# Kernel optimization log

Hardware: AMD Instinct MI355X
Metric: run time of the kernel (lower is better)

## Reference

```python
import jax, jax.numpy as jnp
import numpy as np

N_NODES = 50000
N_EDGES = 800000
N_GRAPHS = 64
F_IN = 128
HEADS = 4
CH = 32
HID = HEADS * CH  # 128
N_CLASSES = 10
N_LAYERS = 3
NEG_SLOPE = 0.2


def setup_inputs() -> dict:
    key = jax.random.key(0)
    ks = jax.random.split(key, 12)
    x = jax.random.normal(ks[0], (N_NODES, F_IN), dtype=jnp.float32)
    edge_index = jax.random.randint(ks[1], (2, N_EDGES), 0, N_NODES, dtype=jnp.int64)
    batch = jnp.sort(jax.random.randint(ks[2], (N_NODES,), 0, N_GRAPHS, dtype=jnp.int64))
    s = 0.1
    Wl = jax.random.normal(ks[3], (N_LAYERS, F_IN, HID), dtype=jnp.float32) * s
    Wr = jax.random.normal(ks[4], (N_LAYERS, F_IN, HID), dtype=jnp.float32) * s
    bl = jax.random.normal(ks[5], (N_LAYERS, HID), dtype=jnp.float32) * s
    br = jax.random.normal(ks[6], (N_LAYERS, HID), dtype=jnp.float32) * s
    att = jax.random.normal(ks[7], (N_LAYERS, HEADS, CH), dtype=jnp.float32) * s
    bias = jax.random.normal(ks[8], (N_LAYERS, HID), dtype=jnp.float32) * s
    lin_w = jax.random.normal(ks[9], (HID, N_CLASSES), dtype=jnp.float32) * s
    lin_b = jax.random.normal(ks[10], (N_CLASSES,), dtype=jnp.float32) * s
    return {"x": x, "edge_index": edge_index, "batch": batch, "Wl": Wl, "Wr": Wr,
            "bl": bl, "br": br, "att": att, "bias": bias, "lin_w": lin_w, "lin_b": lin_b}


def gatv2_layer(x, Wl, Wr, bl, br, att, bias, src, dst):
    # x: [N, D_in] -> out: [N, HEADS*CH]
    n = x.shape[0]
    xl = (x @ Wl + bl).reshape(n, HEADS, CH)  # source transform
    xr = (x @ Wr + br).reshape(n, HEADS, CH)  # target transform
    # GATv2 edge scores: a^T LeakyReLU(W_l x_j + W_r x_i), per head
    e = jnp.einsum('ehc,hc->eh', jax.nn.leaky_relu(xl[src] + xr[dst], NEG_SLOPE), att)  # [E, H]
    # softmax over edges sharing the same destination node
    m = jax.ops.segment_max(e, dst, num_segments=n)
    ee = jnp.exp(e - m[dst])
    denom = jax.ops.segment_sum(ee, dst, num_segments=n)
    alpha = ee / denom[dst]  # [E, H]
    out = jax.ops.segment_sum(xl[src] * alpha[:, :, None], dst, num_segments=n)  # [N, H, C]
    return out.reshape(n, HID) + bias


def reference(x, edge_index, batch, Wl, Wr, bl, br, att, bias, lin_w, lin_b):
    n = x.shape[0]
    loop = jnp.arange(n, dtype=edge_index.dtype)
    src = jnp.concatenate([edge_index[0], loop])  # self loops (PyG default)
    dst = jnp.concatenate([edge_index[1], loop])
    h = x
    for l in range(N_LAYERS):
        h = jax.nn.elu(gatv2_layer(h, Wl[l], Wr[l], bl[l], br[l], att[l], bias[l], src, dst))
    # global mean pool over graphs
    sums = jax.ops.segment_sum(h, batch, num_segments=N_GRAPHS)
    cnt = jax.ops.segment_sum(jnp.ones((n,), h.dtype), batch, num_segments=N_GRAPHS)
    pooled = sums / jnp.maximum(cnt, 1.0)[:, None]
    logits = jax.nn.elu(pooled @ lin_w + lin_b)
    return jax.nn.log_softmax(logits, axis=1)
```

## Files before the change

kernel.cpp:

```cpp
#include <hip/hip_runtime.h>
#include <hip/hip_bf16.h>
#include <math.h>

#define N_NODES 50000
#define N_EDGES 800000
#define N_GRAPHS 64
#define HID 128
#define N_CLASSES 10
#define N_LAYERS 3
#define NEG_SLOPE 0.2f

#define NB 196
#define BCAP 5120
#define ACHUNK 4096

typedef __attribute__((ext_vector_type(8))) short short8;
typedef __attribute__((ext_vector_type(4))) float f32x4;
typedef __attribute__((ext_vector_type(2))) _Float16 h2;

extern "C" __device__ _Float16 __ocml_exp2_f16(_Float16);

__device__ inline ushort f2bf(float f) {
    uint u = __builtin_bit_cast(uint, f);
    u += 0x7fffu + ((u >> 16) & 1u);
    return (ushort)(u >> 16);
}
__device__ inline uint pk2bf(float a, float b) {
    return (uint)f2bf(a) | ((uint)f2bf(b) << 16);
}
__device__ inline h2 pkh(float a, float b) {
    return __builtin_bit_cast(h2, __builtin_amdgcn_cvt_pkrtz(a, b));
}
__device__ inline uint rne8(uint h) {
    return (h + 0x7fu + ((h >> 8) & 1u)) >> 8;
}
__device__ inline uint pk4e5m2(uint h01, uint h23) {
    uint a = rne8(h01 & 0xffffu);
    uint b = rne8(h01 >> 16);
    uint c = rne8(h23 & 0xffffu);
    uint d = rne8(h23 >> 16);
    return a | (b << 8) | (c << 16) | (d << 24);
}


__global__ __launch_bounds__(256) void setup_kernel(
    const float* __restrict__ x, uint* __restrict__ xb, int n,
    const float* __restrict__ Wl, const float* __restrict__ Wr,
    uint* __restrict__ wt, int wtot,
    const int* __restrict__ ei, int E,
    int* __restrict__ bptr, uint* __restrict__ bbuf,
    int xqb, int wb) {
    __shared__ int hcnt[256];
    __shared__ int hexcl[256];
    __shared__ int lofs[256];
    __shared__ int delta[256];
    __shared__ uint stage[ACHUNK];
    int t = threadIdx.x;
    int blk = blockIdx.x;

    if (blk < xqb) {
        int j = blk * 256 + t;
        if (j < n * 16) {
            const float4* xp = (const float4*)x + (size_t)j * 2;
            float4 a = xp[0], b = xp[1];
            uint4 o;
            o.x = pk2bf(a.x, a.y); o.y = pk2bf(a.z, a.w);
            o.z = pk2bf(b.x, b.y); o.w = pk2bf(b.z, b.w);
            ((uint4*)xb)[j] = o;
        }
        return;
    }
    blk -= xqb;
    if (blk < wb) {
        int i = blk * 256 + t;
        if (i >= wtot) return;
        int kp = i & 63;
        int nn = (i >> 6) & 255;
        int l  = i >> 14;
        const float* W = (nn < 128) ? Wl : Wr;
        int c = nn & 127;
        wt[i] = pk2bf(W[l * 16384 + (2 * kp) * 128 + c],
                      W[l * 16384 + (2 * kp + 1) * 128 + c]);
        return;
    }
    blk -= wb;
    int total = E + n;
    int base = blk * ACHUNK;
    int cntblk = min(ACHUNK, total - base);
    hcnt[t] = 0; lofs[t] = 0;
    __syncthreads();

    uint v[16]; int bk[16];
#pragma unroll
    for (int j = 0; j < 16; ++j) {
        int e = base + j * 256 + t;
        bk[j] = -1;
        if (e < total) {
            int s, d;
            if (e < E) { s = ei[e]; d = ei[E + e]; }
            else       { s = e - E; d = e - E; }
            v[j] = ((uint)s << 16) | (uint)d;
            bk[j] = d >> 8;
            atomicAdd(&hcnt[bk[j]], 1);
        }
    }
    __syncthreads();
    int hv = hcnt[t];
    __shared__ int stmp[256];
    stmp[t] = hv;
    __syncthreads();
    for (int off = 1; off < 256; off <<= 1) {
        int u = (t >= off) ? stmp[t - off] : 0;
        __syncthreads();
        stmp[t] += u;
        __syncthreads();
    }
    hexcl[t] = stmp[t] - hv;
    __syncthreads();
#pragma unroll
    for (int j = 0; j < 16; ++j) {
        if (bk[j] >= 0) {
            int pos = hexcl[bk[j]] + atomicAdd(&lofs[bk[j]], 1);
            stage[pos] = v[j];
        }
    }
    __syncthreads();
    if (t < NB) {
        int c = hcnt[t];
        int gb = c ? atomicAdd(&bptr[t], c) : 0;
        delta[t] = t * BCAP + gb - hexcl[t];
    }
    __syncthreads();
    for (int idx = t; idx < cntblk; idx += 256) {
        uint val = stage[idx];
        int b = (val >> 8) & 0xff;
        int tgt = delta[b] + idx;
        if (tgt < (b + 1) * BCAP) bbuf[tgt] = val;
    }
}


__device__ __forceinline__ void gemm_body(
    const ushort* __restrict__ A, const ushort* __restrict__ Wt,
    const float* __restrict__ bl, const float* __restrict__ br,
    uchar* __restrict__ xlb, ushort* __restrict__ xrb, int n, int bid, int tid) {
    int wv = tid >> 6;
    int lane = tid & 63;
    int q = lane >> 4, m16 = lane & 15;
    int m0 = bid * 64;

    short8 bf[4][4];
#pragma unroll
    for (int nt = 0; nt < 4; ++nt) {
        const ushort* wp = Wt + (size_t)(wv * 64 + nt * 16 + m16) * 128 + q * 8;
#pragma unroll
        for (int ks = 0; ks < 4; ++ks) bf[nt][ks] = *(const short8*)(wp + ks * 32);
    }
    const ushort* ap[4];
#pragma unroll
    for (int mt = 0; mt < 4; ++mt) {
        int r = m0 + mt * 16 + m16;
        if (r > n - 1) r = n - 1;
        ap[mt] = A + (size_t)r * 128 + q * 8;
    }

    f32x4 z = {0.f, 0.f, 0.f, 0.f};
    f32x4 acc[4][4];
#pragma unroll
    for (int mt = 0; mt < 4; ++mt)
#pragma unroll
        for (int nt = 0; nt < 4; ++nt) acc[mt][nt] = z;

#pragma unroll
    for (int ks = 0; ks < 4; ++ks) {
        short8 af[4];
#pragma unroll
        for (int mt = 0; mt < 4; ++mt) af[mt] = *(const short8*)(ap[mt] + ks * 32);
#pragma unroll
        for (int mt = 0; mt < 4; ++mt)
#pragma unroll
            for (int nt = 0; nt < 4; ++nt)
                acc[mt][nt] = __builtin_amdgcn_mfma_f32_16x16x32_bf16(
                    bf[nt][ks], af[mt], acc[mt][nt], 0, 0, 0);
    }

    int fb = (wv & 1) * 64;
    if (wv >= 2) {
        const float* bx = br;
#pragma unroll
        for (int nt = 0; nt < 4; ++nt) {
            int fcol = fb + nt * 16 + q * 4;
            float4 b4 = *(const float4*)&bx[fcol];
#pragma unroll
            for (int mt = 0; mt < 4; ++mt) {
                int m = m0 + mt * 16 + m16;
                if (m < n) {
                    uint2 pk;
                    pk.x = __builtin_bit_cast(uint, pkh(acc[mt][nt][0] + b4.x,
                                                        acc[mt][nt][1] + b4.y));
                    pk.y = __builtin_bit_cast(uint, pkh(acc[mt][nt][2] + b4.z,
                                                        acc[mt][nt][3] + b4.w));
                    *(uint2*)&xrb[(size_t)m * 128 + fcol] = pk;
                }
            }
        }
    } else {
        const float* bx = bl;
#pragma unroll
        for (int nt = 0; nt < 4; ++nt) {
            int fcol = fb + nt * 16 + q * 4;
            float4 b4 = *(const float4*)&bx[fcol];
#pragma unroll
            for (int mt = 0; mt < 4; ++mt) {
                int m = m0 + mt * 16 + m16;
                if (m < n) {
                    uint h01 = __builtin_bit_cast(uint, pkh(acc[mt][nt][0] + b4.x,
                                                            acc[mt][nt][1] + b4.y));
                    uint h23 = __builtin_bit_cast(uint, pkh(acc[mt][nt][2] + b4.z,
                                                            acc[mt][nt][3] + b4.w));
                    *(uint*)(xlb + (size_t)m * 128 + fcol) = pk4e5m2(h01, h23);
                }
            }
        }
    }
}

__global__ __launch_bounds__(256) void csr_gemm0_kernel(
    const int* __restrict__ bptr, const uint* __restrict__ bbuf, int n,
    int* __restrict__ row_start, int* __restrict__ ssrc,
    const ushort* __restrict__ A, const ushort* __restrict__ Wt,
    const float* __restrict__ bl, const float* __restrict__ br,
    uchar* __restrict__ xlb, ushort* __restrict__ xrb) {
    int t = threadIdx.x;
    if (blockIdx.x >= NB) {
        gemm_body(A, Wt, bl, br, xlb, xrb, n, blockIdx.x - NB, t);
        return;
    }
    int b = blockIdx.x;
    __shared__ int sb[256], h[256], hx[256], lofs[256];
    int bv = (t < NB) ? min(bptr[t], BCAP) : 0;
    sb[t] = bv;
    __syncthreads();
    for (int off = 1; off < 256; off <<= 1) {
        int u = (t >= off) ? sb[t - off] : 0;
        __syncthreads();
        sb[t] += u;
        __syncthreads();
    }
    int cnt = min(bptr[b], BCAP);
    int base = sb[b] - cnt;
    if (b == NB - 1 && t == 0) row_start[n] = sb[NB - 1];
    h[t] = 0; lofs[t] = 0;
    __syncthreads();
    const uint* bp = bbuf + (size_t)b * BCAP;
    for (int k = t; k < cnt; k += 256) atomicAdd(&h[bp[k] & 255u], 1);
    __syncthreads();
    int hv = h[t];
    hx[t] = hv;
    __syncthreads();
    for (int off = 1; off < 256; off <<= 1) {
        int u = (t >= off) ? hx[t - off] : 0;
        __syncthreads();
        hx[t] += u;
        __syncthreads();
    }
    int excl = hx[t] - hv;
    int node = (b << 8) + t;
    if (node < n) row_start[node] = base + excl;
    __syncthreads();
    h[t] = excl;
    __syncthreads();
    for (int k = t; k < cnt; k += 256) {
        uint val = bp[k];
        int dl = val & 255u;
        int pos = base + h[dl] + atomicAdd(&lofs[dl], 1);
        ssrc[pos] = (int)((val & 0xffff0000u) >> 9);
    }
}

__global__ __launch_bounds__(256) void gemm_mfma(
    const ushort* __restrict__ A, const ushort* __restrict__ Wt,
    const float* __restrict__ bl, const float* __restrict__ br,
    uchar* __restrict__ xlb, ushort* __restrict__ xrb, int n) {
    gemm_body(A, Wt, bl, br, xlb, xrb, n, blockIdx.x, threadIdx.x);
}


#define ESCORE(u, v01, v23, v45, v67, es)                              \
    h2 v01 = __builtin_bit_cast(h2, ((u.x & 0x000000ffu) << 8) |       \
                                    ((u.x & 0x0000ff00u) << 16));      \
    h2 v23 = __builtin_bit_cast(h2, ((u.x >> 8) & 0x0000ff00u) |       \
                                    (u.x & 0xff000000u));              \
    h2 v45 = __builtin_bit_cast(h2, ((u.y & 0x000000ffu) << 8) |       \
                                    ((u.y & 0x0000ff00u) << 16));      \
    h2 v67 = __builtin_bit_cast(h2, ((u.y >> 8) & 0x0000ff00u) |       \
                                    (u.y & 0xff000000u));              \
    _Float16 es;                                                       \
    {                                                                  \
        h2 t01 = v01 + xr01, t23 = v23 + xr23;                         \
        h2 t45 = v45 + xr45, t67 = v67 + xr67;                         \
        t01 = __builtin_elementwise_max(t01, t01 * K02);               \
        t23 = __builtin_elementwise_max(t23, t23 * K02);               \
        t45 = __builtin_elementwise_max(t45, t45 * K02);               \
        t67 = __builtin_elementwise_max(t67, t67 * K02);               \
        h2 eh = EINIT + at01 * t01;                                    \
        eh += at23 * t23;                                              \
        eh += at45 * t45;                                              \
        eh += at67 * t67;                                              \
        es = eh.x + eh.y;                                              \
    }

template <int CTRL>
__device__ inline uint dpp_add_h2(uint q) {
    uint r = (uint)__builtin_amdgcn_mov_dpp((int)q, CTRL, 0xF, 0xF, true);
    h2 s = __builtin_bit_cast(h2, q) + __builtin_bit_cast(h2, r);
    return __builtin_bit_cast(uint, s);
}

__global__ __launch_bounds__(256) void attn_kernel(
    const uchar* __restrict__ xlb, const uint* __restrict__ xrb,
    const float* __restrict__ att, const float* __restrict__ bias,
    const int* __restrict__ row_start, const int* __restrict__ ssrc,
    uint* __restrict__ hout, int n) {
    int wave = threadIdx.x >> 6;
    int lane = threadIdx.x & 63;
    int g    = lane >> 4;
    int l16  = lane & 15;
    int i0n  = blockIdx.x * 16 + wave * 4 + g;
    int i    = min(i0n, n - 1);

    const char* xlB = (const char*)xlb;
    uint lofs8  = (uint)l16 * 8;
    uint lofs16 = (uint)l16 * 16;

    uint4 xru = *(const uint4*)((const char*)xrb + (size_t)i * 256 + lofs16);
    h2 xr01 = __builtin_bit_cast(h2, xru.x);
    h2 xr23 = __builtin_bit_cast(h2, xru.y);
    h2 xr45 = __builtin_bit_cast(h2, xru.z);
    h2 xr67 = __builtin_bit_cast(h2, xru.w);
    const float L2E = 1.4426950408889634f;
    float4 atA = ((const float4*)att)[l16 * 2];
    float4 atB = ((const float4*)att)[l16 * 2 + 1];
    h2 at01 = pkh(atA.x * L2E, atA.y * L2E);
    h2 at23 = pkh(atA.z * L2E, atA.w * L2E);
    h2 at45 = pkh(atB.x * L2E, atB.y * L2E);
    h2 at67 = pkh(atB.z * L2E, atB.w * L2E);
    const h2 K02   = {(_Float16)0.2f, (_Float16)0.2f};
    const h2 EINIT = {(_Float16)-1.0f, (_Float16)-1.0f};

    int p0 = row_start[i], p1 = row_start[i + 1];

    _Float16 denA = (_Float16)0.f, denB = (_Float16)0.f;
    h2 aE01 = {0, 0}, aE23 = {0, 0}, aE45 = {0, 0}, aE67 = {0, 0};
    h2 aO01 = {0, 0}, aO23 = {0, 0}, aO45 = {0, 0}, aO67 = {0, 0};

    int idx = p0;
    uint s0 = (uint)ssrc[idx];
    uint s1 = (uint)ssrc[idx + 1];
    uint s2 = (uint)ssrc[idx + 2];
    uint s3 = (uint)ssrc[idx + 3];
    uint s4 = (uint)ssrc[idx + 4];
    uint s5 = (uint)ssrc[idx + 5];
    uint s6 = (uint)ssrc[idx + 6];
    uint s7 = (uint)ssrc[idx + 7];

    while (idx < p1) {
        uint2 u0 = *(const uint2*)(xlB + s0 + lofs8);
        uint2 u1 = *(const uint2*)(xlB + s1 + lofs8);
        uint2 u2 = *(const uint2*)(xlB + s2 + lofs8);
        uint2 u3 = *(const uint2*)(xlB + s3 + lofs8);
        uint2 u4 = *(const uint2*)(xlB + s4 + lofs8);
        uint2 u5 = *(const uint2*)(xlB + s5 + lofs8);
        uint2 u6 = *(const uint2*)(xlB + s6 + lofs8);
        uint2 u7 = *(const uint2*)(xlB + s7 + lofs8);
        int nidx = idx + 8;
        s0 = (uint)ssrc[nidx];
        s1 = (uint)ssrc[nidx + 1];
        s2 = (uint)ssrc[nidx + 2];
        s3 = (uint)ssrc[nidx + 3];
        s4 = (uint)ssrc[nidx + 4];
        s5 = (uint)ssrc[nidx + 5];
        s6 = (uint)ssrc[nidx + 6];
        s7 = (uint)ssrc[nidx + 7];
        ESCORE(u0, v001, v023, v045, v067, es0);
        ESCORE(u1, v101, v123, v145, v167, es1);
        ESCORE(u2, v201, v223, v245, v267, es2);
        ESCORE(u3, v301, v323, v345, v367, es3);
        ESCORE(u4, v401, v423, v445, v467, es4);
        ESCORE(u5, v501, v523, v545, v567, es5);
        ESCORE(u6, v601, v623, v645, v667, es6);
        ESCORE(u7, v701, v723, v745, v767, es7);
        h2 q01h; q01h.x = es0; q01h.y = es1;
        h2 q23h; q23h.x = es2; q23h.y = es3;
        h2 q45h; q45h.x = es4; q45h.y = es5;
        h2 q67h; q67h.x = es6; q67h.y = es7;
        uint q01 = __builtin_bit_cast(uint, q01h);
        uint q23 = __builtin_bit_cast(uint, q23h);
        uint q45 = __builtin_bit_cast(uint, q45h);
        uint q67 = __builtin_bit_cast(uint, q67h);
        q01 = dpp_add_h2<0xB1>(q01);
        q23 = dpp_add_h2<0xB1>(q23);
        q45 = dpp_add_h2<0xB1>(q45);
        q67 = dpp_add_h2<0xB1>(q67);
        q01 = dpp_add_h2<0x4E>(q01);
        q23 = dpp_add_h2<0x4E>(q23);
        q45 = dpp_add_h2<0x4E>(q45);
        q67 = dpp_add_h2<0x4E>(q67);
        h2 e01 = __builtin_bit_cast(h2, q01);
        h2 e23 = __builtin_bit_cast(h2, q23);
        h2 e45 = __builtin_bit_cast(h2, q45);
        h2 e67 = __builtin_bit_cast(h2, q67);
        const _Float16 zh = (_Float16)0.f;
        _Float16 w0 = (idx     < p1) ? __ocml_exp2_f16(e01.x) : zh;
        _Float16 w1 = (idx + 1 < p1) ? __ocml_exp2_f16(e01.y) : zh;
        _Float16 w2 = (idx + 2 < p1) ? __ocml_exp2_f16(e23.x) : zh;
        _Float16 w3 = (idx + 3 < p1) ? __ocml_exp2_f16(e23.y) : zh;
        _Float16 w4 = (idx + 4 < p1) ? __ocml_exp2_f16(e45.x) : zh;
        _Float16 w5 = (idx + 5 < p1) ? __ocml_exp2_f16(e45.y) : zh;
        _Float16 w6 = (idx + 6 < p1) ? __ocml_exp2_f16(e67.x) : zh;
        _Float16 w7 = (idx + 7 < p1) ? __ocml_exp2_f16(e67.y) : zh;
        denA += w0; denB += w1; denA += w2; denB += w3;
        denA += w4; denB += w5; denA += w6; denB += w7;
        h2 wA = {w0, w0}, wB = {w1, w1}, wC = {w2, w2}, wD = {w3, w3};
        h2 wE = {w4, w4}, wF = {w5, w5}, wG = {w6, w6}, wH = {w7, w7};
        aE01 += wA * v001; aE23 += wA * v023; aE45 += wA * v045; aE67 += wA * v067;
        aO01 += wB * v101; aO23 += wB * v123; aO45 += wB * v145; aO67 += wB * v167;
        aE01 += wC * v201; aE23 += wC * v223; aE45 += wC * v245; aE67 += wC * v267;
        aO01 += wD * v301; aO23 += wD * v323; aO45 += wD * v345; aO67 += wD * v367;
        aE01 += wE * v401; aE23 += wE * v423; aE45 += wE * v445; aE67 += wE * v467;
        aO01 += wF * v501; aO23 += wF * v523; aO45 += wF * v545; aO67 += wF * v567;
        aE01 += wG * v601; aE23 += wG * v623; aE45 += wG * v645; aE67 += wG * v667;
        aO01 += wH * v701; aO23 += wH * v723; aO45 += wH * v745; aO67 += wH * v767;
        idx = nidx;
    }

    float den = (float)denA + (float)denB;
    float inv = 1.f / den;
    h2 a01 = aE01 + aO01;
    h2 a23 = aE23 + aO23;
    h2 a45 = aE45 + aO45;
    h2 a67 = aE67 + aO67;
    float4 biA = ((const float4*)bias)[l16 * 2];
    float4 biB = ((const float4*)bias)[l16 * 2 + 1];
    float o0 = (float)a01.x * inv + biA.x; o0 = o0 > 0.f ? o0 : __expf(o0) - 1.f;
    float o1 = (float)a01.y * inv + biA.y; o1 = o1 > 0.f ? o1 : __expf(o1) - 1.f;
    float o2 = (float)a23.x * inv + biA.z; o2 = o2 > 0.f ? o2 : __expf(o2) - 1.f;
    float o3 = (float)a23.y * inv + biA.w; o3 = o3 > 0.f ? o3 : __expf(o3) - 1.f;
    float o4 = (float)a45.x * inv + biB.x; o4 = o4 > 0.f ? o4 : __expf(o4) - 1.f;
    float o5 = (float)a45.y * inv + biB.y; o5 = o5 > 0.f ? o5 : __expf(o5) - 1.f;
    float o6 = (float)a67.x * inv + biB.z; o6 = o6 > 0.f ? o6 : __expf(o6) - 1.f;
    float o7 = (float)a67.y * inv + biB.w; o7 = o7 > 0.f ? o7 : __expf(o7) - 1.f;
    if (i0n < n) {
        uint4 pk;
        pk.x = pk2bf(o0, o1);
        pk.y = pk2bf(o2, o3);
        pk.z = pk2bf(o4, o5);
        pk.w = pk2bf(o6, o7);
        *(uint4*)((char*)hout + (size_t)i * 256 + lofs16) = pk;
    }
}


__device__ inline float bflo(uint v) { return __builtin_bit_cast(float, v << 16); }
__device__ inline float bfhi(uint v) { return __builtin_bit_cast(float, v & 0xffff0000u); }

__global__ __launch_bounds__(256) void pool_kernel(const uint* __restrict__ h2v,
                                                   const int* __restrict__ batch, int n,
                                                   float* __restrict__ psum) {
    int g = blockIdx.x;
    int t = threadIdx.x;
    int cp = t & 63;
    int sub = (t >> 6) | (blockIdx.y << 2);
    int b, e;
    {
        int lo = 0, hi = n;
        while (lo < hi) { int mid = (lo + hi) >> 1; if (batch[mid] < g) lo = mid + 1; else hi = mid; }
        b = lo;
        lo = 0; hi = n;
        int g1 = g + 1;
        while (lo < hi) { int mid = (lo + hi) >> 1; if (batch[mid] < g1) lo = mid + 1; else hi = mid; }
        e = lo;
    }
    float a0 = 0.f, a1 = 0.f;
    for (int i = b + sub; i < e; i += 32) {
        uint u = h2v[(size_t)i * 64 + cp];
        a0 += bflo(u); a1 += bfhi(u);
    }
    __shared__ float r0[256], r1[256];
    r0[t] = a0; r1[t] = a1;
    __syncthreads();
    if (t < 64) {
        float s0 = r0[t] + r0[t + 64] + r0[t + 128] + r0[t + 192];
        float s1 = r1[t] + r1[t + 64] + r1[t + 128] + r1[t + 192];
        atomicAdd(&psum[g * 128 + 2 * t], s0);
        atomicAdd(&psum[g * 128 + 2 * t + 1], s1);
    }
}

__global__ void final_kernel(const float* __restrict__ psum, const int* __restrict__ batch,
                             int n, const float* __restrict__ lw,
                             const float* __restrict__ lb, float* __restrict__ out) {
    int g = threadIdx.x;
    if (g >= N_GRAPHS) return;
    int b, e;
    {
        int lo = 0, hi = n;
        while (lo < hi) { int mid = (lo + hi) >> 1; if (batch[mid] < g) lo = mid + 1; else hi = mid; }
        b = lo;
        lo = 0; hi = n;
        int g1 = g + 1;
        while (lo < hi) { int mid = (lo + hi) >> 1; if (batch[mid] < g1) lo = mid + 1; else hi = mid; }
        e = lo;
    }
    float invc = 1.f / fmaxf((float)(e - b), 1.f);
    float z[N_CLASSES];
#pragma unroll
    for (int c = 0; c < N_CLASSES; ++c) z[c] = lb[c];
    for (int k = 0; k < 128; ++k) {
        float p = psum[g * 128 + k] * invc;
#pragma unroll
        for (int c = 0; c < N_CLASSES; ++c) z[c] += p * lw[k * N_CLASSES + c];
    }
    float mx = -1e30f;
#pragma unroll
    for (int c = 0; c < N_CLASSES; ++c) {
        z[c] = z[c] > 0.f ? z[c] : expf(z[c]) - 1.f;
        mx = fmaxf(mx, z[c]);
    }
    float s = 0.f;
#pragma unroll
    for (int c = 0; c < N_CLASSES; ++c) s += expf(z[c] - mx);
    float lse = mx + logf(s);
#pragma unroll
    for (int c = 0; c < N_CLASSES; ++c) out[g * N_CLASSES + c] = z[c] - lse;
}


extern "C" void kernel_launch(void* const* d_in, const int* in_sizes, int n_in,
                              void* d_out, int out_size, void* d_ws, size_t ws_size,
                              hipStream_t stream) {
    const float* x     = (const float*)d_in[0];
    const int*   ei    = (const int*)d_in[1];
    const int*   batch = (const int*)d_in[2];
    const float* Wl    = (const float*)d_in[3];
    const float* Wr    = (const float*)d_in[4];
    const float* bl    = (const float*)d_in[5];
    const float* br    = (const float*)d_in[6];
    const float* att   = (const float*)d_in[7];
    const float* bias  = (const float*)d_in[8];
    const float* lw    = (const float*)d_in[9];
    const float* lb    = (const float*)d_in[10];
    float* out = (float*)d_out;

    const int n = in_sizes[2];
    const int E = in_sizes[1] / 2;
    const int total_edges = E + n;

    char* ws = (char*)d_ws;
    size_t o = 0;
    auto alloc = [&](size_t bytes) -> void* {
        void* p = ws + o;
        o = (o + bytes + 255) & ~(size_t)255;
        return p;
    };
    int*    row_start = (int*)alloc((size_t)(n + 1) * 4);
    int*    bptr      = (int*)alloc((size_t)NB * 4);
    uint*   bbuf      = (uint*)alloc((size_t)NB * BCAP * 4);
    int*    ssrc      = (int*)alloc((size_t)(total_edges + 64) * 4);
    ushort* xbf0      = (ushort*)alloc((size_t)n * HID * 2);
    uchar*  xlb       = (uchar*)alloc((size_t)n * HID);
    ushort* xrb       = (ushort*)alloc((size_t)n * HID * 2);
    ushort* hbA       = (ushort*)alloc((size_t)n * HID * 2);
    ushort* hbB       = (ushort*)alloc((size_t)n * HID * 2);
    uint*   wt        = (uint*)alloc((size_t)N_LAYERS * 256 * 64 * 4);
    float*  psum      = (float*)alloc((size_t)N_GRAPHS * HID * 4);

    hipMemsetAsync(bptr, 0, (size_t)NB * 4, stream);
    hipMemsetAsync(psum, 0, (size_t)N_GRAPHS * HID * 4, stream);
    hipMemsetAsync(ssrc + total_edges, 0, 64 * 4, stream);

    int wtot = N_LAYERS * 256 * 64;
    int xqb = (n * 16 + 255) / 256;
    int wb  = (wtot + 255) / 256;
    int pb  = (total_edges + ACHUNK - 1) / ACHUNK;
    setup_kernel<<<xqb + wb + pb, 256, 0, stream>>>(
        x, (uint*)xbf0, n, Wl, Wr, wt, wtot, ei, E, bptr, bbuf, xqb, wb);

    int mblocks = (n + 63) / 64;
    int ablocks = (n + 15) / 16;

    csr_gemm0_kernel<<<NB + mblocks, 256, 0, stream>>>(
        bptr, bbuf, n, row_start, ssrc,
        xbf0, (const ushort*)wt, bl, br, xlb, xrb);

    attn_kernel<<<ablocks, 256, 0, stream>>>(xlb, (const uint*)xrb,
                                             att, bias, row_start, ssrc, (uint*)hbA, n);
    gemm_mfma<<<mblocks, 256, 0, stream>>>(hbA, (const ushort*)(wt + (size_t)256 * 64),
                                           bl + HID, br + HID, xlb, xrb, n);
    attn_kernel<<<ablocks, 256, 0, stream>>>(xlb, (const uint*)xrb,
                                             att + HID, bias + HID, row_start, ssrc,
                                             (uint*)hbB, n);
    gemm_mfma<<<mblocks, 256, 0, stream>>>(hbB, (const ushort*)(wt + (size_t)2 * 256 * 64),
                                           bl + 2 * HID, br + 2 * HID, xlb, xrb, n);
    attn_kernel<<<ablocks, 256, 0, stream>>>(xlb, (const uint*)xrb,
                                             att + 2 * HID, bias + 2 * HID, row_start, ssrc,
                                             (uint*)hbA, n);

    pool_kernel<<<dim3(N_GRAPHS, 8), 256, 0, stream>>>((const uint*)hbA, batch, n, psum);
    final_kernel<<<1, 64, 0, stream>>>(psum, batch, n, lw, lb, out);
}
```

Before: 322.4 us.

## Fuse x conversion into first GEMM and mean pooling into last attention

The first-layer GEMM now reads fp32 x directly and converts it to bf16 in registers, so the setup pass no longer writes an intermediate bf16 copy of x. The last attention layer accumulates its outputs into per-graph sums through shared-memory atomics, falling back to global atomics, which removes the bf16 store of the final hidden state and the separate pool kernel. The final classifier kernel is spread over 256 threads with a shared-memory reduction. In exchange, the first GEMM loads twice the bytes per A fragment, and the pooling path adds many atomic operations inside the attention kernel.

```diff
diff --git a/kernel.cpp b/kernel.cpp
--- a/kernel.cpp
+++ b/kernel.cpp
@@ -44,12 +44,10 @@
 
 
 __global__ __launch_bounds__(256) void setup_kernel(
-    const float* __restrict__ x, uint* __restrict__ xb, int n,
     const float* __restrict__ Wl, const float* __restrict__ Wr,
     uint* __restrict__ wt, int wtot,
-    const int* __restrict__ ei, int E,
-    int* __restrict__ bptr, uint* __restrict__ bbuf,
-    int xqb, int wb) {
+    const int* __restrict__ ei, int E, int n,
+    int* __restrict__ bptr, uint* __restrict__ bbuf, int wb) {
     __shared__ int hcnt[256];
     __shared__ int hexcl[256];
     __shared__ int lofs[256];
@@ -58,19 +56,6 @@
     int t = threadIdx.x;
     int blk = blockIdx.x;
 
-    if (blk < xqb) {
-        int j = blk * 256 + t;
-        if (j < n * 16) {
-            const float4* xp = (const float4*)x + (size_t)j * 2;
-            float4 a = xp[0], b = xp[1];
-            uint4 o;
-            o.x = pk2bf(a.x, a.y); o.y = pk2bf(a.z, a.w);
-            o.z = pk2bf(b.x, b.y); o.w = pk2bf(b.z, b.w);
-            ((uint4*)xb)[j] = o;
-        }
-        return;
-    }
-    blk -= xqb;
     if (blk < wb) {
         int i = blk * 256 + t;
         if (i >= wtot) return;
@@ -140,8 +125,9 @@
 }
 
 
+template <bool AF32>
 __device__ __forceinline__ void gemm_body(
-    const ushort* __restrict__ A, const ushort* __restrict__ Wt,
+    const void* __restrict__ Av, const ushort* __restrict__ Wt,
     const float* __restrict__ bl, const float* __restrict__ br,
     uchar* __restrict__ xlb, ushort* __restrict__ xrb, int n, int bid, int tid) {
     int wv = tid >> 6;
@@ -156,12 +142,13 @@
 #pragma unroll
         for (int ks = 0; ks < 4; ++ks) bf[nt][ks] = *(const short8*)(wp + ks * 32);
     }
-    const ushort* ap[4];
+    const char* abase = (const char*)Av;
+    const char* ap[4];
 #pragma unroll
     for (int mt = 0; mt < 4; ++mt) {
         int r = m0 + mt * 16 + m16;
         if (r > n - 1) r = n - 1;
-        ap[mt] = A + (size_t)r * 128 + q * 8;
+        ap[mt] = abase + (size_t)r * (AF32 ? 512 : 256) + q * (AF32 ? 32 : 16);
     }
 
     f32x4 z = {0.f, 0.f, 0.f, 0.f};
@@ -175,7 +162,18 @@
     for (int ks = 0; ks < 4; ++ks) {
         short8 af[4];
 #pragma unroll
-        for (int mt = 0; mt < 4; ++mt) af[mt] = *(const short8*)(ap[mt] + ks * 32);
+        for (int mt = 0; mt < 4; ++mt) {
+            if constexpr (AF32) {
+                const float4* p = (const float4*)(ap[mt] + ks * 128);
+                float4 a = p[0], b = p[1];
+                uint4 u;
+                u.x = pk2bf(a.x, a.y); u.y = pk2bf(a.z, a.w);
+                u.z = pk2bf(b.x, b.y); u.w = pk2bf(b.z, b.w);
+                af[mt] = __builtin_bit_cast(short8, u);
+            } else {
+                af[mt] = *(const short8*)(ap[mt] + ks * 64);
+            }
+        }
 #pragma unroll
         for (int mt = 0; mt < 4; ++mt)
 #pragma unroll
@@ -228,12 +226,12 @@
 __global__ __launch_bounds__(256) void csr_gemm0_kernel(
     const int* __restrict__ bptr, const uint* __restrict__ bbuf, int n,
     int* __restrict__ row_start, int* __restrict__ ssrc,
-    const ushort* __restrict__ A, const ushort* __restrict__ Wt,
+    const float* __restrict__ x, const ushort* __restrict__ Wt,
     const float* __restrict__ bl, const float* __restrict__ br,
     uchar* __restrict__ xlb, ushort* __restrict__ xrb) {
     int t = threadIdx.x;
     if (blockIdx.x >= NB) {
-        gemm_body(A, Wt, bl, br, xlb, xrb, n, blockIdx.x - NB, t);
+        gemm_body<true>((const void*)x, Wt, bl, br, xlb, xrb, n, blockIdx.x - NB, t);
         return;
     }
     int b = blockIdx.x;
@@ -282,7 +280,7 @@
     const ushort* __restrict__ A, const ushort* __restrict__ Wt,
     const float* __restrict__ bl, const float* __restrict__ br,
     uchar* __restrict__ xlb, ushort* __restrict__ xrb, int n) {
-    gemm_body(A, Wt, bl, br, xlb, xrb, n, blockIdx.x, threadIdx.x);
+    gemm_body<false>((const void*)A, Wt, bl, br, xlb, xrb, n, blockIdx.x, threadIdx.x);
 }
 
 
@@ -317,17 +315,29 @@
     return __builtin_bit_cast(uint, s);
 }
 
+template <bool POOL>
 __global__ __launch_bounds__(256) void attn_kernel(
     const uchar* __restrict__ xlb, const uint* __restrict__ xrb,
     const float* __restrict__ att, const float* __restrict__ bias,
     const int* __restrict__ row_start, const int* __restrict__ ssrc,
-    uint* __restrict__ hout, int n) {
+    uint* __restrict__ hout, const int* __restrict__ batch,
+    float* __restrict__ psum, int n) {
+    __shared__ float sacc[4][128];
+    __shared__ int used[4];
     int wave = threadIdx.x >> 6;
     int lane = threadIdx.x & 63;
     int g    = lane >> 4;
     int l16  = lane & 15;
     int i0n  = blockIdx.x * 16 + wave * 4 + g;
     int i    = min(i0n, n - 1);
+
+    int gmin = 0;
+    if constexpr (POOL) {
+        gmin = batch[blockIdx.x * 16];
+        for (int k = threadIdx.x; k < 512; k += 256) ((float*)sacc)[k] = 0.f;
+        if (threadIdx.x < 4) used[threadIdx.x] = 0;
+        __syncthreads();
+    }
 
     const char* xlB = (const char*)xlb;
     uint lofs8  = (uint)l16 * 8;
@@ -450,27 +460,60 @@
     float o5 = (float)a45.y * inv + biB.y; o5 = o5 > 0.f ? o5 : __expf(o5) - 1.f;
     float o6 = (float)a67.x * inv + biB.z; o6 = o6 > 0.f ? o6 : __expf(o6) - 1.f;
     float o7 = (float)a67.y * inv + biB.w; o7 = o7 > 0.f ? o7 : __expf(o7) - 1.f;
-    if (i0n < n) {
-        uint4 pk;
-        pk.x = pk2bf(o0, o1);
-        pk.y = pk2bf(o2, o3);
-        pk.z = pk2bf(o4, o5);
-        pk.w = pk2bf(o6, o7);
-        *(uint4*)((char*)hout + (size_t)i * 256 + lofs16) = pk;
-    }
-}
-
-
-__device__ inline float bflo(uint v) { return __builtin_bit_cast(float, v << 16); }
-__device__ inline float bfhi(uint v) { return __builtin_bit_cast(float, v & 0xffff0000u); }
-
-__global__ __launch_bounds__(256) void pool_kernel(const uint* __restrict__ h2v,
-                                                   const int* __restrict__ batch, int n,
-                                                   float* __restrict__ psum) {
-    int g = blockIdx.x;
+
+    if constexpr (POOL) {
+        if (i0n < n) {
+            int gb = batch[i];
+            int slot = gb - gmin;
+            int c0 = l16 * 8;
+            if (slot < 4) {
+                if (l16 == 0) used[slot] = 1;
+                atomicAdd(&sacc[slot][c0 + 0], o0);
+                atomicAdd(&sacc[slot][c0 + 1], o1);
+                atomicAdd(&sacc[slot][c0 + 2], o2);
+                atomicAdd(&sacc[slot][c0 + 3], o3);
+                atomicAdd(&sacc[slot][c0 + 4], o4);
+                atomicAdd(&sacc[slot][c0 + 5], o5);
+                atomicAdd(&sacc[slot][c0 + 6], o6);
+                atomicAdd(&sacc[slot][c0 + 7], o7);
+            } else {
+                atomicAdd(&psum[gb * 128 + c0 + 0], o0);
+                atomicAdd(&psum[gb * 128 + c0 + 1], o1);
+                atomicAdd(&psum[gb * 128 + c0 + 2], o2);
+                atomicAdd(&psum[gb * 128 + c0 + 3], o3);
+                atomicAdd(&psum[gb * 128 + c0 + 4], o4);
+                atomicAdd(&psum[gb * 128 + c0 + 5], o5);
+                atomicAdd(&psum[gb * 128 + c0 + 6], o6);
+                atomicAdd(&psum[gb * 128 + c0 + 7], o7);
+            }
+        }
+        __syncthreads();
+        for (int k = threadIdx.x; k < 512; k += 256) {
+            int s = k >> 7, c = k & 127;
+            if (used[s]) {
+                float v = sacc[s][c];
+                if (v != 0.f) atomicAdd(&psum[(gmin + s) * 128 + c], v);
+            }
+        }
+    } else {
+        if (i0n < n) {
+            uint4 pk;
+            pk.x = pk2bf(o0, o1);
+            pk.y = pk2bf(o2, o3);
+            pk.z = pk2bf(o4, o5);
+            pk.w = pk2bf(o6, o7);
+            *(uint4*)((char*)hout + (size_t)i * 256 + lofs16) = pk;
+        }
+    }
+}
+
+
+__global__ __launch_bounds__(256) void final_kernel(
+    const float* __restrict__ psum, const int* __restrict__ batch, int n,
+    const float* __restrict__ lw, const float* __restrict__ lb,
+    float* __restrict__ out) {
     int t = threadIdx.x;
-    int cp = t & 63;
-    int sub = (t >> 6) | (blockIdx.y << 2);
+    int g = t >> 2, q = t & 3;
     int b, e;
     {
         int lo = 0, hi = n;
@@ -481,58 +524,39 @@
         while (lo < hi) { int mid = (lo + hi) >> 1; if (batch[mid] < g1) lo = mid + 1; else hi = mid; }
         e = lo;
     }
-    float a0 = 0.f, a1 = 0.f;
-    for (int i = b + sub; i < e; i += 32) {
-        uint u = h2v[(size_t)i * 64 + cp];
-        a0 += bflo(u); a1 += bfhi(u);
-    }
-    __shared__ float r0[256], r1[256];
-    r0[t] = a0; r1[t] = a1;
-    __syncthreads();
-    if (t < 64) {
-        float s0 = r0[t] + r0[t + 64] + r0[t + 128] + r0[t + 192];
-        float s1 = r1[t] + r1[t + 64] + r1[t + 128] + r1[t + 192];
-        atomicAdd(&psum[g * 128 + 2 * t], s0);
-        atomicAdd(&psum[g * 128 + 2 * t + 1], s1);
-    }
-}
-
-__global__ void final_kernel(const float* __restrict__ psum, const int* __restrict__ batch,
-                             int n, const float* __restrict__ lw,
-                             const float* __restrict__ lb, float* __restrict__ out) {
-    int g = threadIdx.x;
-    if (g >= N_GRAPHS) return;
-    int b, e;
-    {
-        int lo = 0, hi = n;
-        while (lo < hi) { int mid = (lo + hi) >> 1; if (batch[mid] < g) lo = mid + 1; else hi = mid; }
-        b = lo;
-        lo = 0; hi = n;
-        int g1 = g + 1;
-        while (lo < hi) { int mid = (lo + hi) >> 1; if (batch[mid] < g1) lo = mid + 1; else hi = mid; }
-        e = lo;
-    }
     float invc = 1.f / fmaxf((float)(e - b), 1.f);
     float z[N_CLASSES];
 #pragma unroll
-    for (int c = 0; c < N_CLASSES; ++c) z[c] = lb[c];
-    for (int k = 0; k < 128; ++k) {
-        float p = psum[g * 128 + k] * invc;
-#pragma unroll
-        for (int c = 0; c < N_CLASSES; ++c) z[c] += p * lw[k * N_CLASSES + c];
-    }
-    float mx = -1e30f;
-#pragma unroll
-    for (int c = 0; c < N_CLASSES; ++c) {
-        z[c] = z[c] > 0.f ? z[c] : expf(z[c]) - 1.f;
-        mx = fmaxf(mx, z[c]);
-    }
-    float s = 0.f;
-#pragma unroll
-    for (int c = 0; c < N_CLASSES; ++c) s += expf(z[c] - mx);
-    float lse = mx + logf(s);
-#pragma unroll
-    for (int c = 0; c < N_CLASSES; ++c) out[g * N_CLASSES + c] = z[c] - lse;
+    for (int c = 0; c < N_CLASSES; ++c) z[c] = 0.f;
+    const float* ps = psum + g * 128 + q * 32;
+    const float* lwp = lw + (q * 32) * N_CLASSES;
+#pragma unroll 4
+    for (int k = 0; k < 32; ++k) {
+        float p = ps[k] * invc;
+#pragma unroll
+        for (int c = 0; c < N_CLASSES; ++c) z[c] += p * lwp[k * N_CLASSES + c];
+    }
+    __shared__ float red[64][4][N_CLASSES];
+#pragma unroll
+    for (int c = 0; c < N_CLASSES; ++c) red[g][q][c] = z[c];
+    __syncthreads();
+    if (q == 0) {
+#pragma unroll
+        for (int c = 0; c < N_CLASSES; ++c)
+            z[c] = red[g][0][c] + red[g][1][c] + red[g][2][c] + red[g][3][c] + lb[c];
+        float mx = -1e30f;
+#pragma unroll
+        for (int c = 0; c < N_CLASSES; ++c) {
+            z[c] = z[c] > 0.f ? z[c] : expf(z[c]) - 1.f;
+            mx = fmaxf(mx, z[c]);
+        }
+        float s = 0.f;
+#pragma unroll
+        for (int c = 0; c < N_CLASSES; ++c) s += expf(z[c] - mx);
+        float lse = mx + logf(s);
+#pragma unroll
+        for (int c = 0; c < N_CLASSES; ++c) out[g * N_CLASSES + c] = z[c] - lse;
+    }
 }
 
 
@@ -567,7 +591,6 @@
     int*    bptr      = (int*)alloc((size_t)NB * 4);
     uint*   bbuf      = (uint*)alloc((size_t)NB * BCAP * 4);
     int*    ssrc      = (int*)alloc((size_t)(total_edges + 64) * 4);
-    ushort* xbf0      = (ushort*)alloc((size_t)n * HID * 2);
     uchar*  xlb       = (uchar*)alloc((size_t)n * HID);
     ushort* xrb       = (ushort*)alloc((size_t)n * HID * 2);
     ushort* hbA       = (ushort*)alloc((size_t)n * HID * 2);
@@ -580,32 +603,31 @@
     hipMemsetAsync(ssrc + total_edges, 0, 64 * 4, stream);
 
     int wtot = N_LAYERS * 256 * 64;
-    int xqb = (n * 16 + 255) / 256;
     int wb  = (wtot + 255) / 256;
     int pb  = (total_edges + ACHUNK - 1) / ACHUNK;
-    setup_kernel<<<xqb + wb + pb, 256, 0, stream>>>(
-        x, (uint*)xbf0, n, Wl, Wr, wt, wtot, ei, E, bptr, bbuf, xqb, wb);
+    setup_kernel<<<wb + pb, 256, 0, stream>>>(
+        Wl, Wr, wt, wtot, ei, E, n, bptr, bbuf, wb);
 
     int mblocks = (n + 63) / 64;
     int ablocks = (n + 15) / 16;
 
     csr_gemm0_kernel<<<NB + mblocks, 256, 0, stream>>>(
         bptr, bbuf, n, row_start, ssrc,
-        xbf0, (const ushort*)wt, bl, br, xlb, xrb);
-
-    attn_kernel<<<ablocks, 256, 0, stream>>>(xlb, (const uint*)xrb,
-                                             att, bias, row_start, ssrc, (uint*)hbA, n);
+        x, (const ushort*)wt, bl, br, xlb, xrb);
+
+    attn_kernel<false><<<ablocks, 256, 0, stream>>>(
+        xlb, (const uint*)xrb, att, bias, row_start, ssrc,
+        (uint*)hbA, nullptr, nullptr, n);
     gemm_mfma<<<mblocks, 256, 0, stream>>>(hbA, (const ushort*)(wt + (size_t)256 * 64),
                                            bl + HID, br + HID, xlb, xrb, n);
-    attn_kernel<<<ablocks, 256, 0, stream>>>(xlb, (const uint*)xrb,
-                                             att + HID, bias + HID, row_start, ssrc,
-                                             (uint*)hbB, n);
+    attn_kernel<false><<<ablocks, 256, 0, stream>>>(
+        xlb, (const uint*)xrb, att + HID, bias + HID, row_start, ssrc,
+        (uint*)hbB, nullptr, nullptr, n);
     gemm_mfma<<<mblocks, 256, 0, stream>>>(hbB, (const ushort*)(wt + (size_t)2 * 256 * 64),
                                            bl + 2 * HID, br + 2 * HID, xlb, xrb, n);
-    attn_kernel<<<ablocks, 256, 0, stream>>>(xlb, (const uint*)xrb,
-                                             att + 2 * HID, bias + 2 * HID, row_start, ssrc,
-                                             (uint*)hbA, n);
-
-    pool_kernel<<<dim3(N_GRAPHS, 8), 256, 0, stream>>>((const uint*)hbA, batch, n, psum);
-    final_kernel<<<1, 64, 0, stream>>>(psum, batch, n, lw, lb, out);
-}
+    attn_kernel<true><<<ablocks, 256, 0, stream>>>(
+        xlb, (const uint*)xrb, att + 2 * HID, bias + 2 * HID, row_start, ssrc,
+        nullptr, batch, psum, n);
+
+    final_kernel<<<1, 256, 0, stream>>>(psum, batch, n, lw, lb, out);
+}
```

Result: slower. 329.3 us (+2.1%).
